# Kernel tuning notes

Hardware: AMD Instinct MI355X
Metric: run time of the kernel (lower is better)

## Reference

```python
import jax, jax.numpy as jnp
import numpy as np
import math

HIDDEN = 768
HEADS = 12
HEAD_DIM = HIDDEN // HEADS
BLOCK = 256
TOPK = 3
BATCH = 2
SEQ = 2048


def setup_inputs() -> dict:
    key = jax.random.key(0)
    ks = jax.random.split(key, 5)
    s = 1.0 / math.sqrt(HIDDEN)
    return {
        "hidden_states": jax.random.normal(ks[0], (BATCH, SEQ, HIDDEN), jnp.float32),
        "Wq": jax.random.normal(ks[1], (HIDDEN, HIDDEN), jnp.float32) * s,
        "Wk": jax.random.normal(ks[2], (HIDDEN, HIDDEN), jnp.float32) * s,
        "Wv": jax.random.normal(ks[3], (HIDDEN, HIDDEN), jnp.float32) * s,
        "Wo": jax.random.normal(ks[4], (HIDDEN, HIDDEN), jnp.float32) * s,
    }


def _rope(x, sin, cos):
    # x: [B, H, S, D]; rotate-half RoPE
    d2 = x.shape[-1] // 2
    x1, x2 = x[..., :d2], x[..., d2:]
    return x * cos + jnp.concatenate([-x2, x1], axis=-1) * sin


def reference(hidden_states, Wq, Wk, Wv, Wo):
    B, S, Hd = hidden_states.shape
    H, D, bs, K = HEADS, HEAD_DIM, BLOCK, TOPK
    nb = S // bs  # number of key blocks
    scale = 1.0 / math.sqrt(D)

    def split_heads(x):
        return x.reshape(B, S, H, D).transpose(0, 2, 1, 3)  # [B,H,S,D]

    q = split_heads(hidden_states @ Wq.T)
    k = split_heads(hidden_states @ Wk.T)
    v = split_heads(hidden_states @ Wv.T)

    # rotary embedding (standard rotate-half RoPE, base 10000)
    inv_freq = 1.0 / (10000.0 ** (jnp.arange(0, D, 2, dtype=jnp.float32) / D))
    ang = jnp.arange(S, dtype=jnp.float32)[:, None] * inv_freq[None, :]  # [S, D/2]
    emb = jnp.concatenate([ang, ang], axis=-1)  # [S, D]
    sin, cos = jnp.sin(emb), jnp.cos(emb)
    q = _rope(q, sin, cos)
    k = _rope(k, sin, cos)

    # mean-pooled block representations of keys: [B,H,nb,D]
    block_reps = k.reshape(B, H, nb, bs, D).mean(axis=3)

    # routing scores: per-token score against each block rep
    bscores = jnp.einsum('bhsd,bhnd->bhsn', q, block_reps) * scale  # [B,H,S,nb]
    pos = jnp.arange(S)
    cur = pos // bs                       # current block of each query, [S]
    blk = jnp.arange(nb)
    future = blk[None, None, None, :] > cur[None, None, :, None]
    bscores = jnp.where(future, -jnp.inf, bscores)
    # current block is force-selected (score set to dtype max)
    is_cur = blk[None, None, None, :] == cur[None, None, :, None]
    bscores = jnp.where(is_cur, jnp.finfo(bscores.dtype).max, bscores)

    _, topk_idx = jax.lax.top_k(bscores, min(K, nb))  # [B,H,S,K]
    selected = jnp.sum(jax.nn.one_hot(topk_idx, nb, dtype=jnp.float32), axis=-2) > 0  # [B,H,S,nb]

    # per-key-position mask: key t allowed iff its block is selected for query i,
    # and within the current block only t <= i (matches original truncation).
    sel_t = selected[:, :, :, cur]                          # [B,H,Sq,Sk]
    intra_ok = (cur[None, :] != cur[:, None]) | (pos[None, :] <= pos[:, None])  # [Sq,Sk]
    mask = sel_t & intra_ok[None, None]

    scores = jnp.einsum('bhqd,bhkd->bhqk', q, k) * scale
    scores = jnp.where(mask, scores, -jnp.inf)
    probs = jax.nn.softmax(scores, axis=-1)
    out = jnp.einsum('bhqk,bhkd->bhqd', probs, v)

    out = out.transpose(0, 2, 1, 3).reshape(B, S, Hd)
    return out @ Wo.T
```

## Files before the change

### kernel.cpp

```cpp
#include <hip/hip_runtime.h>
#include <math.h>


#define HID   768
#define NH    12
#define DH    64
#define SEQN  2048
#define BATCH 2
#define NTOK  (BATCH*SEQN)
#define NB    8
#define BLKSZ 256
#define NEG_INF (-__builtin_huge_valf())
#define POS_INF (__builtin_huge_valf())
#define LO_SCALE 2048.0f
#define LO_INV   (1.0f/2048.0f)
#define EXP2C    0.18033688f

typedef unsigned short u16;
typedef _Float16 v8hf __attribute__((ext_vector_type(8)));
typedef float    v4f  __attribute__((ext_vector_type(4)));

__device__ __forceinline__ u16 f2h(float x) {
    _Float16 h = (_Float16)x;
    return __builtin_bit_cast(u16, h);
}
__device__ __forceinline__ float h2f(u16 u) {
    return (float)__builtin_bit_cast(_Float16, u);
}
__device__ __forceinline__ v8hf ldhf8(const u16* p) {
    return *reinterpret_cast<const v8hf*>(p);
}
__device__ __forceinline__ void g2lds16(const u16* g, u16* l) {
    __builtin_amdgcn_global_load_lds(
        (const __attribute__((address_space(1))) void*)g,
        (__attribute__((address_space(3))) void*)l, 16, 0, 0);
}
#define MFMA16(a, b, c) __builtin_amdgcn_mfma_f32_16x16x32_f16(a, b, c, 0, 0, 0)

__global__ __launch_bounds__(256)
void preproc_k(const float* __restrict__ X,  const float* __restrict__ Wq,
               const float* __restrict__ Wk, const float* __restrict__ Wv,
               const float* __restrict__ Wo, float2* __restrict__ tab,
               u16* __restrict__ Xh, u16* __restrict__ Xl,
               u16* __restrict__ Wq2, u16* __restrict__ Wk2,
               u16* __restrict__ Wv2, u16* __restrict__ Wo2)
{
    const int NW = HID * HID;
    const int id = blockIdx.x;
    const int tid = threadIdx.x;
    if (id < 12288) {
        const int i = id * 256 + tid;
        const float x = X[i];
        const u16 h = f2h(x);
        Xh[i] = h;
        Xl[i] = f2h((x - h2f(h)) * LO_SCALE);
    } else if (id < 21504) {
        const int j = (id - 12288) * 256 + tid;
        const int z = j / NW, i = j - z * NW;
        const float* src = (z == 0) ? Wq : (z == 1) ? Wk : (z == 2) ? Wv : Wo;
        u16* dst = (z == 0) ? Wq2 : (z == 1) ? Wk2 : (z == 2) ? Wv2 : Wo2;
        const float x = src[i];
        const u16 h = f2h(x);
        dst[i] = h;
        dst[i + NW] = f2h((x - h2f(h)) * LO_SCALE);
    } else {
        const int i = (id - 21504) * 256 + tid;
        const int s = i >> 5, f = i & 31;
        const double y  = exp((double)f * (log(10000.0) / 32.0));
        const float yf = (float)y;
        const float invf = 1.0f / yf;
        const float ang  = (float)s * invf;
        tab[i] = make_float2((float)sin((double)ang), (float)cos((double)ang));
    }
}

__device__ __forceinline__
void qkv_mainloop(const u16* __restrict__ Ah, const u16* __restrict__ Al,
                  const u16* __restrict__ Bh, const u16* __restrict__ Bl,
                  int m0, int nb0, int c_start,
                  u16* As, u16* Bs, v4f acc[2][4])
{
    const int tid = threadIdx.x;
    const int w = tid >> 6, lane = tid & 63;
    const int col = lane & 15, quad = lane >> 4;

    int a_row[4], a_gl[4];
    #pragma unroll
    for (int r = 0; r < 4; r++) {
        const int g = r * 256 + tid;
        a_row[r] = g >> 3;
        a_gl[r]  = (g & 7) ^ (a_row[r] & 7);
    }
    int b_row[2], b_gl[2];
    #pragma unroll
    for (int r = 0; r < 2; r++) {
        const int g = r * 256 + tid;
        b_row[r] = g >> 3;
        b_gl[r]  = (g & 7) ^ (b_row[r] & 7);
    }

    for (int c = c_start; c < 3; c++) {
        const u16* Ap = (c == 0) ? Al : Ah;
        const u16* Bp = (c == 1) ? Bl : Bh;
        for (int itc = 0; itc < HID / 64; itc++) {
            const int k0 = itc * 64;
            __syncthreads();
            #pragma unroll
            for (int r = 0; r < 4; r++)
                g2lds16(Ap + (size_t)(m0 + a_row[r]) * HID + k0 + a_gl[r] * 8,
                        &As[(r * 256 + w * 64) * 8]);
            #pragma unroll
            for (int r = 0; r < 2; r++)
                g2lds16(Bp + (size_t)(nb0 + b_row[r]) * HID + k0 + b_gl[r] * 8,
                        &Bs[(r * 256 + w * 64) * 8]);
            __syncthreads();
            #pragma unroll
            for (int ks = 0; ks < 2; ks++) {
                v8hf af[2], bf_[4];
                #pragma unroll
                for (int mt = 0; mt < 2; mt++) {
                    const int row = w * 32 + mt * 16 + col;
                    const int gph = (ks * 4 + quad) ^ (row & 7);
                    af[mt] = ldhf8(&As[row * 64 + gph * 8]);
                }
                #pragma unroll
                for (int nt = 0; nt < 4; nt++) {
                    const int row = nt * 16 + col;
                    const int gph = (ks * 4 + quad) ^ (row & 7);
                    bf_[nt] = ldhf8(&Bs[row * 64 + gph * 8]);
                }
                #pragma unroll
                for (int mt = 0; mt < 2; mt++)
                    #pragma unroll
                    for (int nt = 0; nt < 4; nt++)
                        acc[mt][nt] = MFMA16(af[mt], bf_[nt], acc[mt][nt]);
            }
        }
        if (c == 1) {
            #pragma unroll
            for (int mt = 0; mt < 2; mt++)
                #pragma unroll
                for (int nt = 0; nt < 4; nt++)
                    #pragma unroll
                    for (int r = 0; r < 4; r++)
                        acc[mt][nt][r] *= LO_INV;
        }
    }
    __syncthreads();
}

__global__ __launch_bounds__(256)
void qkv_fused_gemm_k(const u16* __restrict__ Xh, const u16* __restrict__ Xl,
                      const u16* __restrict__ Wq2, const u16* __restrict__ Wk2,
                      const u16* __restrict__ Wv2, const float2* __restrict__ tab,
                      float* __restrict__ q32, u16* __restrict__ kh16,
                      u16* __restrict__ vth, float* __restrict__ partial)
{
    __shared__ u16 As[128 * 64];
    __shared__ u16 Bs[64 * 64];
    __shared__ float psum[4][64];

    const int NW = HID * HID;
    const int id    = blockIdx.x;
    const int xcd   = id & 7, loc = id >> 3;
    const int mtile = xcd * 4 + (loc & 3);
    const int ntile = loc >> 2;
    const int m0  = mtile * 128;
    const int mat = ntile / 12;
    const int nb0 = (ntile - mat * 12) * 64;
    const u16* Bh = (mat == 0) ? Wq2 : (mat == 1) ? Wk2 : Wv2;

    v4f acc[2][4] = {};
    qkv_mainloop(Xh, Xl, Bh, Bh + NW, m0, nb0, (mat == 2) ? 1 : 0, As, Bs, acc);

    const int tid = threadIdx.x;
    const int w = tid >> 6, lane = tid & 63;
    const int col = lane & 15, quad = lane >> 4;
    const int b = m0 >> 11;
    const int h = nb0 >> 6;
    const size_t bh = (size_t)b * NH + h;

    if (mat == 2) {
        #pragma unroll
        for (int nt = 0; nt < 4; nt++) {
            const int d = nt * 16 + col;
            #pragma unroll
            for (int mt = 0; mt < 2; mt++) {
                const int m = m0 + w * 32 + mt * 16 + quad * 4;
                const int s = m & (SEQN - 1);
                ushort4 pk = make_ushort4(f2h(acc[mt][nt][0]), f2h(acc[mt][nt][1]),
                                          f2h(acc[mt][nt][2]), f2h(acc[mt][nt][3]));
                *(ushort4*)&vth[(bh * DH + d) * SEQN + s] = pk;
            }
        }
        return;
    }

    float vsum[4] = {0.f, 0.f, 0.f, 0.f};
    #pragma unroll
    for (int mt = 0; mt < 2; mt++) {
        #pragma unroll
        for (int nt = 0; nt < 4; nt++) {
            const int d = nt * 16 + col;
            #pragma unroll
            for (int r = 0; r < 4; r++) {
                const int m = m0 + w * 32 + mt * 16 + quad * 4 + r;
                const int s = m & (SEQN - 1);
                const float part = acc[mt][nt ^ 2][r];
                const float2 sc = tab[(s << 5) + (d & 31)];
                const float val = (d < 32) ? acc[mt][nt][r] * sc.y - part * sc.x
                                           : acc[mt][nt][r] * sc.y + part * sc.x;
                const size_t idx = (bh * SEQN + s) * DH + d;
                if (mat == 0) {
                    q32[idx] = val;
                } else {
                    kh16[idx] = f2h(val);
                    vsum[nt] += val;
                }
            }
        }
    }
    if (mat == 1) {
        #pragma unroll
        for (int nt = 0; nt < 4; nt++) {
            float v = vsum[nt];
            v += __shfl_xor(v, 16);
            v += __shfl_xor(v, 32);
            if (quad == 0) psum[w][nt * 16 + col] = v;
        }
        __syncthreads();
        if (tid < 64) {
            const float s4 = (psum[0][tid] + psum[1][tid])
                           + (psum[2][tid] + psum[3][tid]);
            const int nblk = (m0 & (SEQN - 1)) >> 8;
            const int half = (m0 >> 7) & 1;
            partial[((bh * NB + nblk) * 2 + half) * 64 + tid] = s4;
        }
    }
}

__global__ __launch_bounds__(256)
void out_gemm_mfma_k(const u16* __restrict__ Ah, const u16* __restrict__ Wo2,
                     float* __restrict__ C)
{
    __shared__ u16 As[64 * 64];
    __shared__ u16 Bs[64 * 64];

    const int NW = HID * HID;
    const int id    = blockIdx.x;
    const int xcd   = id & 7, loc = id >> 3;
    const int mtile = xcd * 8 + (loc & 7);
    const int ntile = loc >> 3;
    const int m0 = mtile * 64, n0 = ntile * 64;
    const int tid = threadIdx.x;
    const int w = tid >> 6, lane = tid & 63;
    const int col = lane & 15, quad = lane >> 4;

    const int r0 = tid >> 3,         gl0 = (tid & 7) ^ (r0 & 7);
    const int r1 = (256 + tid) >> 3, gl1 = ((256 + tid) & 7) ^ (r1 & 7);

    v4f acc[4] = {};
    #pragma unroll
    for (int c = 0; c < 2; c++) {
        const u16* Bp = (c == 0) ? (Wo2 + NW) : Wo2;
        for (int itc = 0; itc < HID / 64; itc++) {
            const int k0 = itc * 64;
            __syncthreads();
            g2lds16(Ah + (size_t)(m0 + r0) * HID + k0 + gl0 * 8, &As[(w * 64) * 8]);
            g2lds16(Ah + (size_t)(m0 + r1) * HID + k0 + gl1 * 8, &As[(256 + w * 64) * 8]);
            g2lds16(Bp + (size_t)(n0 + r0) * HID + k0 + gl0 * 8, &Bs[(w * 64) * 8]);
            g2lds16(Bp + (size_t)(n0 + r1) * HID + k0 + gl1 * 8, &Bs[(256 + w * 64) * 8]);
            __syncthreads();
            #pragma unroll
            for (int ks = 0; ks < 2; ks++) {
                const int arow = w * 16 + col;
                v8hf a = ldhf8(&As[arow * 64 + (((ks * 4 + quad) ^ (arow & 7))) * 8]);
                #pragma unroll
                for (int nt = 0; nt < 4; nt++) {
                    const int row = nt * 16 + col;
                    v8hf bb = ldhf8(&Bs[row * 64 + (((ks * 4 + quad) ^ (row & 7))) * 8]);
                    acc[nt] = MFMA16(a, bb, acc[nt]);
                }
            }
        }
        if (c == 0) {
            #pragma unroll
            for (int nt = 0; nt < 4; nt++)
                #pragma unroll
                for (int r = 0; r < 4; r++)
                    acc[nt][r] *= LO_INV;
        }
    }

    #pragma unroll
    for (int nt = 0; nt < 4; nt++)
        #pragma unroll
        for (int r = 0; r < 4; r++) {
            const int m = m0 + w * 16 + quad * 4 + r;
            C[(size_t)m * HID + n0 + nt * 16 + col] = acc[nt][r];
        }
}

__global__ __launch_bounds__(64)
void reps_reduce_k(const float* __restrict__ partial, float* __restrict__ reps)
{
    const int bhn = blockIdx.x;
    const int d = threadIdx.x;
    const float* p = &partial[(size_t)bhn * 128 + d];
    double s = (double)p[0] + (double)p[64];
    reps[(size_t)bhn * 64 + d] = (float)(s * (1.0 / 256.0));
}

__global__ __launch_bounds__(128)
void select_topk_k(const float* __restrict__ qg, const float* __restrict__ reps,
                   unsigned* __restrict__ selm)
{
    __shared__ float rs[NB][DH];
    const int bh = blockIdx.y;
    const int tid = threadIdx.x;
    for (int idx = tid; idx < NB * DH; idx += 128)
        rs[idx >> 6][idx & 63] = reps[(size_t)bh * NB * DH + idx];
    __syncthreads();

    const int qq = blockIdx.x * 128 + tid;
    const float* qv = &qg[((size_t)bh * SEQN + qq) * DH];
    float qr[DH];
    #pragma unroll
    for (int c = 0; c < 16; c++) {
        float4 t = *(const float4*)&qv[c * 4];
        qr[c*4+0]=t.x; qr[c*4+1]=t.y; qr[c*4+2]=t.z; qr[c*4+3]=t.w;
    }
    const int cur = qq >> 8;
    double sc[NB];
    #pragma unroll
    for (int n = 0; n < NB; n++) {
        double ssum = 0.0;
        for (int d = 0; d < DH; d++) ssum += (double)qr[d] * (double)rs[n][d];
        sc[n] = ssum * 0.125;
    }
    for (int n = cur + 1; n < NB; n++) sc[n] = -1e300;
    sc[cur] = 1e300;
    unsigned mask = 0;
    for (int p = 0; p < 3; p++) {
        int bi = -1; double bv = 0.0;
        for (int n = 0; n < NB; n++) {
            if ((mask >> n) & 1) continue;
            if (bi < 0 || sc[n] > bv) { bi = n; bv = sc[n]; }
        }
        mask |= 1u << bi;
    }
    selm[(size_t)bh * SEQN + qq] = mask;
}

__global__ __launch_bounds__(256, 4)
void moba_attn_k(const float* __restrict__ q32, const u16* __restrict__ kh16,
                 const u16* __restrict__ vth, const unsigned* __restrict__ selm,
                 u16* __restrict__ aoh)
{
    __shared__ u16 kbuf[2][64 * 64];
    __shared__ u16 vbuf[2][64 * 64];
    __shared__ u16 plds[4][16][64];
    unsigned* s_uni = (unsigned*)&vbuf[1][0];

    const int id  = blockIdx.x;
    const int xcd = id & 7, loc = id >> 3;
    const int bh  = xcd * 3 + (loc >> 5);
    const int q0  = (loc & 31) * 64;
    const int cur = q0 >> 8;
    const int tid = threadIdx.x;
    const int wave = tid >> 6, lane = tid & 63;
    const int col = lane & 15, quad = lane >> 4;
    const int qw0 = q0 + wave * 16;
    const int qpos = qw0 + col;
    const size_t bhS = (size_t)bh * SEQN;
    const size_t bhV = (size_t)bh * DH;

    if (tid == 0) *s_uni = 0;
    __syncthreads();
    const unsigned mymask = selm[bhS + qw0 + col];
    unsigned uw = mymask;
    #pragma unroll
    for (int off = 1; off < 16; off <<= 1) uw |= __shfl_xor(uw, off);
    if (lane == 0) atomicOr(s_uni, uw);

    v8hf qh[2], ql[2];
    #pragma unroll
    for (int ks = 0; ks < 2; ks++) {
        const float* qp = &q32[(bhS + qw0 + col) * DH + ks * 32 + quad * 8];
        float4 f0 = *(const float4*)qp;
        float4 f1 = *(const float4*)(qp + 4);
        float qf[8] = {f0.x, f0.y, f0.z, f0.w, f1.x, f1.y, f1.z, f1.w};
        union { u16 u[8]; v8hf h; } uh, ul;
        #pragma unroll
        for (int j = 0; j < 8; j++) {
            u16 hb = f2h(qf[j]);
            uh.u[j] = hb;
            ul.u[j] = f2h((qf[j] - h2f(hb)) * LO_SCALE);
        }
        qh[ks] = uh.h; ql[ks] = ul.h;
    }
    __syncthreads();
    const unsigned uni = __builtin_amdgcn_readfirstlane(*s_uni);

    int n_cur = __builtin_ctz(uni), c_cur = 0;
    int n_nxt = n_cur, c_nxt = 0;
    bool has_nxt = true;
    auto c2max = [&](int n) { return (n == cur) ? ((q0 + 63 - n * BLKSZ) >> 6) : 3; };
    auto advance = [&]() {
        if (c_nxt < c2max(n_nxt)) { c_nxt++; return; }
        has_nxt = false;
        for (int nn = n_nxt + 1; nn < NB; nn++)
            if ((uni >> nn) & 1) { n_nxt = nn; c_nxt = 0; has_nxt = true; return; }
    };
    advance();

    const int sg_row0 = tid >> 3;
    const int sg_gl0  = (tid & 7) ^ (sg_row0 & 7);
    const int sg_row1 = (256 + tid) >> 3;
    const int sg_gl1  = ((256 + tid) & 7) ^ (sg_row1 & 7);
    auto stage = [&](int n, int c2, int buf) {
        const int kb = n * BLKSZ + c2 * 64;
        u16* kd = (u16*)kbuf[buf];
        u16* vd = (u16*)vbuf[buf];
        const size_t ks0 = (bhS + kb + sg_row0) * DH + sg_gl0 * 8;
        const size_t ks1 = (bhS + kb + sg_row1) * DH + sg_gl1 * 8;
        const size_t vs0 = (bhV + sg_row0) * SEQN + kb + sg_gl0 * 8;
        const size_t vs1 = (bhV + sg_row1) * SEQN + kb + sg_gl1 * 8;
        g2lds16(kh16 + ks0, kd + (wave * 64) * 8);
        g2lds16(kh16 + ks1, kd + (256 + wave * 64) * 8);
        g2lds16(vth + vs0, vd + (wave * 64) * 8);
        g2lds16(vth + vs1, vd + (256 + wave * 64) * 8);
    };

    const v4f zero4 = {0.f, 0.f, 0.f, 0.f};
    v4f oacc[4] = {zero4, zero4, zero4, zero4};
    float m_i = NEG_INF, l_i = 0.f;
    const int psw = (col & 7) << 1;

    stage(n_cur, c_cur, 0);
    int t = 0;
    while (true) {
        __syncthreads();
        if (has_nxt) stage(n_nxt, c_nxt, (t + 1) & 1);

        const int n  = n_cur;
        const int kb = n * BLKSZ + c_cur * 64;
        const bool iscur = (n == cur);
        const float selinf = ((mymask >> n) & 1) ? 0.f : POS_INF;
        const bool need_mask = iscur && (kb + 63 > qw0);
        const u16* kd = (const u16*)kbuf[t & 1];
        const u16* vd = (const u16*)vbuf[t & 1];

        v4f sf[4];
        #pragma unroll
        for (int mt = 0; mt < 4; mt++) {
            const int row = mt * 16 + col;
            const int r7 = row & 7;
            v8hf kh0 = ldhf8(&kd[(row * 8 + (quad ^ r7)) * 8]);
            v8hf kh1 = ldhf8(&kd[(row * 8 + ((4 + quad) ^ r7)) * 8]);
            v4f c = zero4;
            c = MFMA16(kh0, ql[0], c);
            c = MFMA16(kh1, ql[1], c);
            #pragma unroll
            for (int r = 0; r < 4; r++) c[r] *= LO_INV;
            c = MFMA16(kh0, qh[0], c);
            c = MFMA16(kh1, qh[1], c);
            sf[mt] = c;
        }

        if (need_mask) {
            #pragma unroll
            for (int mt = 0; mt < 4; mt++)
                #pragma unroll
                for (int r = 0; r < 4; r++) {
                    const int kidx = kb + mt * 16 + quad * 4 + r;
                    sf[mt][r] = (kidx <= qpos) ? sf[mt][r] : NEG_INF;
                }
        }

        float rm = NEG_INF;
        #pragma unroll
        for (int mt = 0; mt < 4; mt++)
            #pragma unroll
            for (int r = 0; r < 4; r++) rm = fmaxf(rm, sf[mt][r]);
        rm = fmaxf(rm, __shfl_xor(rm, 16));
        rm = fmaxf(rm, __shfl_xor(rm, 32));
        rm = rm - selinf;
        const float mnew  = fmaxf(m_i, rm);
        const float alpha = (m_i == NEG_INF) ? 0.f : exp2f((m_i - mnew) * EXP2C);
        const float biasC = ((mnew == NEG_INF) ? 0.f : mnew * EXP2C) + selinf;

        float lsum = 0.f;
        #pragma unroll
        for (int mt = 0; mt < 4; mt++) {
            ushort4 hv;
            #pragma unroll
            for (int r = 0; r < 4; r++) {
                float p = exp2f(fmaf(sf[mt][r], EXP2C, -biasC));
                lsum += p;
                u16 hu = f2h(p);
                if (r == 0) hv.x = hu;
                else if (r == 1) hv.y = hu;
                else if (r == 2) hv.z = hu;
                else hv.w = hu;
            }
            *(ushort4*)&plds[wave][col][((mt * 4 + quad) ^ psw) * 4] = hv;
        }
        lsum += __shfl_xor(lsum, 16);
        lsum += __shfl_xor(lsum, 32);
        l_i = l_i * alpha + lsum;
        m_i = mnew;

        float ar[4];
        #pragma unroll
        for (int r = 0; r < 4; r++) ar[r] = __shfl(alpha, quad * 4 + r, 16);
        #pragma unroll
        for (int nt = 0; nt < 4; nt++)
            #pragma unroll
            for (int r = 0; r < 4; r++) oacc[nt][r] *= ar[r];

        __threadfence_block();

        #pragma unroll
        for (int ks2 = 0; ks2 < 2; ks2++) {
            v8hf ph = ldhf8(&plds[wave][col][((ks2 * 8 + quad * 2) ^ psw) * 4]);
            #pragma unroll
            for (int nt = 0; nt < 4; nt++) {
                const int row = nt * 16 + col;
                const int g = (ks2 * 4 + quad) ^ (row & 7);
                v8hf vh = ldhf8(&vd[(row * 8 + g) * 8]);
                oacc[nt] = MFMA16(ph, vh, oacc[nt]);
            }
        }

        if (!has_nxt) break;
        n_cur = n_nxt; c_cur = c_nxt;
        advance();
        t++;
    }

    const int b = bh / NH, h = bh % NH;
    const float invl = 1.f / l_i;
    float ir[4];
    #pragma unroll
    for (int r = 0; r < 4; r++) ir[r] = __shfl(invl, quad * 4 + r, 16);
    #pragma unroll
    for (int nt = 0; nt < 4; nt++)
        #pragma unroll
        for (int r = 0; r < 4; r++) {
            const int qi = qw0 + quad * 4 + r;
            const size_t idx = ((size_t)b * SEQN + qi) * HID + h * DH + nt * 16 + col;
            aoh[idx] = f2h(oacc[nt][r] * ir[r]);
        }
}

extern "C" void kernel_launch(void* const* d_in, const int* in_sizes, int n_in,
                              void* d_out, int out_size, void* d_ws, size_t ws_size,
                              hipStream_t stream)
{
    const float* X  = (const float*)d_in[0];
    const float* Wq = (const float*)d_in[1];
    const float* Wk = (const float*)d_in[2];
    const float* Wv = (const float*)d_in[3];
    const float* Wo = (const float*)d_in[4];
    float* out = (float*)d_out;

    char* p = (char*)d_ws;
    float* q32 = (float*)p;                p += (size_t)NTOK*HID*4;
    u16* kh16 = (u16*)p;                   p += (size_t)NTOK*HID*2;
    u16* vth  = (u16*)p;                   p += (size_t)NTOK*HID*2;
    u16* Xh   = (u16*)p;                   p += (size_t)NTOK*HID*2;
    u16* Xl   = (u16*)p;                   p += (size_t)NTOK*HID*2;
    u16* Wq2  = (u16*)p;                   p += (size_t)HID*HID*2*2;
    u16* Wk2  = (u16*)p;                   p += (size_t)HID*HID*2*2;
    u16* Wv2  = (u16*)p;                   p += (size_t)HID*HID*2*2;
    u16* Wo2  = (u16*)p;                   p += (size_t)HID*HID*2*2;
    float* partial = (float*)p;            p += (size_t)BATCH*NH*NB*2*64*4;
    float* reps    = (float*)p;            p += (size_t)BATCH*NH*NB*DH*4;
    unsigned* selm = (unsigned*)p;         p += (size_t)BATCH*NH*SEQN*4;
    float2* tab    = (float2*)p;           p += (size_t)SEQN*32*8;
    u16* aoh = Xh;

    preproc_k<<<dim3(21760), 256, 0, stream>>>(X, Wq, Wk, Wv, Wo, tab,
                                               Xh, Xl, Wq2, Wk2, Wv2, Wo2);

    qkv_fused_gemm_k<<<dim3(1152), 256, 0, stream>>>(
        Xh, Xl, Wq2, Wk2, Wv2, tab, q32, kh16, vth, partial);

    reps_reduce_k<<<dim3(BATCH*NH*NB), 64, 0, stream>>>(partial, reps);
    select_topk_k<<<dim3(SEQN/128, BATCH*NH), 128, 0, stream>>>(q32, reps, selm);

    moba_attn_k<<<dim3(BATCH*NH*(SEQN/64)), 256, 0, stream>>>(
        q32, kh16, vth, selm, aoh);

    out_gemm_mfma_k<<<dim3(768), 256, 0, stream>>>(aoh, Wo2, out);
}
```

Measured before the change: 235.5 us.

## Split attention KV loop for late query blocks and merge partials in combine kernel

```diff
diff --git a/kernel.cpp b/kernel.cpp
--- a/kernel.cpp
+++ b/kernel.cpp
@@ -15,6 +15,9 @@
 #define LO_SCALE 2048.0f
 #define LO_INV   (1.0f/2048.0f)
 #define EXP2C    0.18033688f
+
+#define SPLIT_ROWS 1024
+#define NBH   (BATCH*NH)
 
 typedef unsigned short u16;
 typedef _Float16 v8hf __attribute__((ext_vector_type(8)));
@@ -355,7 +358,8 @@
 __global__ __launch_bounds__(256, 4)
 void moba_attn_k(const float* __restrict__ q32, const u16* __restrict__ kh16,
                  const u16* __restrict__ vth, const unsigned* __restrict__ selm,
-                 u16* __restrict__ aoh)
+                 u16* __restrict__ aoh, float* __restrict__ po,
+                 float* __restrict__ ml)
 {
     __shared__ u16 kbuf[2][64 * 64];
     __shared__ u16 vbuf[2][64 * 64];
@@ -364,8 +368,12 @@
 
     const int id  = blockIdx.x;
     const int xcd = id & 7, loc = id >> 3;
-    const int bh  = xcd * 3 + (loc >> 5);
-    const int q0  = (loc & 31) * 64;
+    const int bh  = xcd * 3 + loc / 48;
+    const int u   = loc % 48;
+    int qb, split, stride;
+    if (u < 16) { qb = u;                 split = 0;          stride = 1; }
+    else        { qb = 16 + ((u - 16) >> 1); split = (u - 16) & 1; stride = 2; }
+    const int q0  = qb * 64;
     const int cur = q0 >> 8;
     const int tid = threadIdx.x;
     const int wave = tid >> 6, lane = tid & 63;
@@ -382,6 +390,7 @@
     #pragma unroll
     for (int off = 1; off < 16; off <<= 1) uw |= __shfl_xor(uw, off);
     if (lane == 0) atomicOr(s_uni, uw);
+    const unsigned wmask = __builtin_amdgcn_readfirstlane(uw);
 
     v8hf qh[2], ql[2];
     #pragma unroll
@@ -402,17 +411,39 @@
     __syncthreads();
     const unsigned uni = __builtin_amdgcn_readfirstlane(*s_uni);
 
-    int n_cur = __builtin_ctz(uni), c_cur = 0;
-    int n_nxt = n_cur, c_nxt = 0;
+    int n_nxt = __builtin_ctz(uni), c_nxt = 0;
     bool has_nxt = true;
     auto c2max = [&](int n) { return (n == cur) ? ((q0 + 63 - n * BLKSZ) >> 6) : 3; };
-    auto advance = [&]() {
+    auto advance1 = [&]() {
         if (c_nxt < c2max(n_nxt)) { c_nxt++; return; }
+        for (int nn = n_nxt + 1; nn < NB; nn++)
+            if ((uni >> nn) & 1) { n_nxt = nn; c_nxt = 0; return; }
         has_nxt = false;
-        for (int nn = n_nxt + 1; nn < NB; nn++)
-            if ((uni >> nn) & 1) { n_nxt = nn; c_nxt = 0; has_nxt = true; return; }
     };
-    advance();
+    for (int i = 0; i < split; i++) if (has_nxt) advance1();
+    int n_cur = n_nxt, c_cur = c_nxt;
+    const bool cur_valid = has_nxt;
+
+    const size_t srow0 = (size_t)bh * SPLIT_ROWS + (q0 - SPLIT_ROWS);
+
+    if (!cur_valid) {
+        if (stride == 2) {
+            if (quad == 0) {
+                const size_t r = srow0 + wave * 16 + col;
+                ml[(r * 2 + split) * 2 + 0] = NEG_INF;
+                ml[(r * 2 + split) * 2 + 1] = 0.f;
+            }
+            #pragma unroll
+            for (int nt = 0; nt < 4; nt++)
+                #pragma unroll
+                for (int r = 0; r < 4; r++) {
+                    const size_t rq = srow0 + wave * 16 + quad * 4 + r;
+                    po[(rq * 2 + split) * 64 + nt * 16 + col] = 0.f;
+                }
+        }
+        return;
+    }
+    for (int i = 0; i < stride; i++) if (has_nxt) advance1();
 
     const int sg_row0 = tid >> 3;
     const int sg_gl0  = (tid & 7) ^ (sg_row0 & 7);
@@ -444,99 +475,121 @@
         if (has_nxt) stage(n_nxt, c_nxt, (t + 1) & 1);
 
         const int n  = n_cur;
-        const int kb = n * BLKSZ + c_cur * 64;
-        const bool iscur = (n == cur);
-        const float selinf = ((mymask >> n) & 1) ? 0.f : POS_INF;
-        const bool need_mask = iscur && (kb + 63 > qw0);
-        const u16* kd = (const u16*)kbuf[t & 1];
-        const u16* vd = (const u16*)vbuf[t & 1];
-
-        v4f sf[4];
-        #pragma unroll
-        for (int mt = 0; mt < 4; mt++) {
-            const int row = mt * 16 + col;
-            const int r7 = row & 7;
-            v8hf kh0 = ldhf8(&kd[(row * 8 + (quad ^ r7)) * 8]);
-            v8hf kh1 = ldhf8(&kd[(row * 8 + ((4 + quad) ^ r7)) * 8]);
-            v4f c = zero4;
-            c = MFMA16(kh0, ql[0], c);
-            c = MFMA16(kh1, ql[1], c);
-            #pragma unroll
-            for (int r = 0; r < 4; r++) c[r] *= LO_INV;
-            c = MFMA16(kh0, qh[0], c);
-            c = MFMA16(kh1, qh[1], c);
-            sf[mt] = c;
-        }
-
-        if (need_mask) {
+        if ((wmask >> n) & 1) {
+            const int kb = n * BLKSZ + c_cur * 64;
+            const bool iscur = (n == cur);
+            const float selinf = ((mymask >> n) & 1) ? 0.f : POS_INF;
+            const bool need_mask = iscur && (kb + 63 > qw0);
+            const u16* kd = (const u16*)kbuf[t & 1];
+            const u16* vd = (const u16*)vbuf[t & 1];
+
+            v4f sf[4];
+            __builtin_amdgcn_s_setprio(1);
+            #pragma unroll
+            for (int mt = 0; mt < 4; mt++) {
+                const int row = mt * 16 + col;
+                const int r7 = row & 7;
+                v8hf kh0 = ldhf8(&kd[(row * 8 + (quad ^ r7)) * 8]);
+                v8hf kh1 = ldhf8(&kd[(row * 8 + ((4 + quad) ^ r7)) * 8]);
+                v4f c = zero4;
+                c = MFMA16(kh0, ql[0], c);
+                c = MFMA16(kh1, ql[1], c);
+                #pragma unroll
+                for (int r = 0; r < 4; r++) c[r] *= LO_INV;
+                c = MFMA16(kh0, qh[0], c);
+                c = MFMA16(kh1, qh[1], c);
+                sf[mt] = c;
+            }
+            __builtin_amdgcn_s_setprio(0);
+
+            if (need_mask) {
+                #pragma unroll
+                for (int mt = 0; mt < 4; mt++)
+                    #pragma unroll
+                    for (int r = 0; r < 4; r++) {
+                        const int kidx = kb + mt * 16 + quad * 4 + r;
+                        sf[mt][r] = (kidx <= qpos) ? sf[mt][r] : NEG_INF;
+                    }
+            }
+
+            float rm = NEG_INF;
             #pragma unroll
             for (int mt = 0; mt < 4; mt++)
                 #pragma unroll
+                for (int r = 0; r < 4; r++) rm = fmaxf(rm, sf[mt][r]);
+            rm = fmaxf(rm, __shfl_xor(rm, 16));
+            rm = fmaxf(rm, __shfl_xor(rm, 32));
+            rm = rm - selinf;
+            const float mnew  = fmaxf(m_i, rm);
+            const float alpha = (m_i == NEG_INF) ? 0.f : exp2f((m_i - mnew) * EXP2C);
+            const float biasC = ((mnew == NEG_INF) ? 0.f : mnew * EXP2C) + selinf;
+
+            float lsum = 0.f;
+            #pragma unroll
+            for (int mt = 0; mt < 4; mt++) {
+                ushort4 hv;
+                #pragma unroll
                 for (int r = 0; r < 4; r++) {
-                    const int kidx = kb + mt * 16 + quad * 4 + r;
-                    sf[mt][r] = (kidx <= qpos) ? sf[mt][r] : NEG_INF;
+                    float p = exp2f(fmaf(sf[mt][r], EXP2C, -biasC));
+                    lsum += p;
+                    u16 hu = f2h(p);
+                    if (r == 0) hv.x = hu;
+                    else if (r == 1) hv.y = hu;
+                    else if (r == 2) hv.z = hu;
+                    else hv.w = hu;
                 }
-        }
-
-        float rm = NEG_INF;
-        #pragma unroll
-        for (int mt = 0; mt < 4; mt++)
-            #pragma unroll
-            for (int r = 0; r < 4; r++) rm = fmaxf(rm, sf[mt][r]);
-        rm = fmaxf(rm, __shfl_xor(rm, 16));
-        rm = fmaxf(rm, __shfl_xor(rm, 32));
-        rm = rm - selinf;
-        const float mnew  = fmaxf(m_i, rm);
-        const float alpha = (m_i == NEG_INF) ? 0.f : exp2f((m_i - mnew) * EXP2C);
-        const float biasC = ((mnew == NEG_INF) ? 0.f : mnew * EXP2C) + selinf;
-
-        float lsum = 0.f;
-        #pragma unroll
-        for (int mt = 0; mt < 4; mt++) {
-            ushort4 hv;
-            #pragma unroll
-            for (int r = 0; r < 4; r++) {
-                float p = exp2f(fmaf(sf[mt][r], EXP2C, -biasC));
-                lsum += p;
-                u16 hu = f2h(p);
-                if (r == 0) hv.x = hu;
-                else if (r == 1) hv.y = hu;
-                else if (r == 2) hv.z = hu;
-                else hv.w = hu;
-            }
-            *(ushort4*)&plds[wave][col][((mt * 4 + quad) ^ psw) * 4] = hv;
-        }
-        lsum += __shfl_xor(lsum, 16);
-        lsum += __shfl_xor(lsum, 32);
-        l_i = l_i * alpha + lsum;
-        m_i = mnew;
-
-        float ar[4];
-        #pragma unroll
-        for (int r = 0; r < 4; r++) ar[r] = __shfl(alpha, quad * 4 + r, 16);
+                *(ushort4*)&plds[wave][col][((mt * 4 + quad) ^ psw) * 4] = hv;
+            }
+            lsum += __shfl_xor(lsum, 16);
+            lsum += __shfl_xor(lsum, 32);
+            l_i = l_i * alpha + lsum;
+            m_i = mnew;
+
+            float ar[4];
+            #pragma unroll
+            for (int r = 0; r < 4; r++) ar[r] = __shfl(alpha, quad * 4 + r, 16);
+            #pragma unroll
+            for (int nt = 0; nt < 4; nt++)
+                #pragma unroll
+                for (int r = 0; r < 4; r++) oacc[nt][r] *= ar[r];
+
+            __threadfence_block();
+
+            __builtin_amdgcn_s_setprio(1);
+            #pragma unroll
+            for (int ks2 = 0; ks2 < 2; ks2++) {
+                v8hf ph = ldhf8(&plds[wave][col][((ks2 * 8 + quad * 2) ^ psw) * 4]);
+                #pragma unroll
+                for (int nt = 0; nt < 4; nt++) {
+                    const int row = nt * 16 + col;
+                    const int g = (ks2 * 4 + quad) ^ (row & 7);
+                    v8hf vh = ldhf8(&vd[(row * 8 + g) * 8]);
+                    oacc[nt] = MFMA16(ph, vh, oacc[nt]);
+                }
+            }
+            __builtin_amdgcn_s_setprio(0);
+        }
+
+        if (!has_nxt) break;
+        n_cur = n_nxt; c_cur = c_nxt;
+        for (int i = 0; i < stride; i++) if (has_nxt) advance1();
+        t++;
+    }
+
+    if (stride == 2) {
+        if (quad == 0) {
+            const size_t r = srow0 + wave * 16 + col;
+            ml[(r * 2 + split) * 2 + 0] = m_i;
+            ml[(r * 2 + split) * 2 + 1] = l_i;
+        }
         #pragma unroll
         for (int nt = 0; nt < 4; nt++)
             #pragma unroll
-            for (int r = 0; r < 4; r++) oacc[nt][r] *= ar[r];
-
-        __threadfence_block();
-
-        #pragma unroll
-        for (int ks2 = 0; ks2 < 2; ks2++) {
-            v8hf ph = ldhf8(&plds[wave][col][((ks2 * 8 + quad * 2) ^ psw) * 4]);
-            #pragma unroll
-            for (int nt = 0; nt < 4; nt++) {
-                const int row = nt * 16 + col;
-                const int g = (ks2 * 4 + quad) ^ (row & 7);
-                v8hf vh = ldhf8(&vd[(row * 8 + g) * 8]);
-                oacc[nt] = MFMA16(ph, vh, oacc[nt]);
-            }
-        }
-
-        if (!has_nxt) break;
-        n_cur = n_nxt; c_cur = c_nxt;
-        advance();
-        t++;
+            for (int r = 0; r < 4; r++) {
+                const size_t rq = srow0 + wave * 16 + quad * 4 + r;
+                po[(rq * 2 + split) * 64 + nt * 16 + col] = oacc[nt][r];
+            }
+        return;
     }
 
     const int b = bh / NH, h = bh % NH;
@@ -552,6 +605,28 @@
             const size_t idx = ((size_t)b * SEQN + qi) * HID + h * DH + nt * 16 + col;
             aoh[idx] = f2h(oacc[nt][r] * ir[r]);
         }
+}
+
+__global__ __launch_bounds__(256)
+void attn_combine_k(const float* __restrict__ po, const float* __restrict__ ml,
+                    u16* __restrict__ aoh)
+{
+    const int g = blockIdx.x * 256 + threadIdx.x;
+    const int d = g & 63;
+    const size_t row = (size_t)(g >> 6);
+    const int bh = (int)(row >> 10);
+    const int qlocal = (int)(row & 1023);
+    const float m0 = ml[(row * 2 + 0) * 2 + 0], l0 = ml[(row * 2 + 0) * 2 + 1];
+    const float m1 = ml[(row * 2 + 1) * 2 + 0], l1 = ml[(row * 2 + 1) * 2 + 1];
+    const float m  = fmaxf(m0, m1);
+    const float a0 = (m0 == NEG_INF) ? 0.f : exp2f((m0 - m) * EXP2C);
+    const float a1 = (m1 == NEG_INF) ? 0.f : exp2f((m1 - m) * EXP2C);
+    const float o  = po[(row * 2 + 0) * 64 + d] * a0
+                   + po[(row * 2 + 1) * 64 + d] * a1;
+    const float inv = 1.f / (l0 * a0 + l1 * a1);
+    const int b = bh / NH, h = bh % NH;
+    const int q = SPLIT_ROWS + qlocal;
+    aoh[((size_t)b * SEQN + q) * HID + h * DH + d] = f2h(o * inv);
 }
 
 extern "C" void kernel_launch(void* const* d_in, const int* in_sizes, int n_in,
@@ -581,6 +656,9 @@
     float2* tab    = (float2*)p;           p += (size_t)SEQN*32*8;
     u16* aoh = Xh;
 
+    float* po = (float*)Xl;
+    float* ml = po + (size_t)NBH * SPLIT_ROWS * 2 * 64;
+
     preproc_k<<<dim3(21760), 256, 0, stream>>>(X, Wq, Wk, Wv, Wo, tab,
                                                Xh, Xl, Wq2, Wk2, Wv2, Wo2);
 
@@ -590,8 +668,10 @@
     reps_reduce_k<<<dim3(BATCH*NH*NB), 64, 0, stream>>>(partial, reps);
     select_topk_k<<<dim3(SEQN/128, BATCH*NH), 128, 0, stream>>>(q32, reps, selm);
 
-    moba_attn_k<<<dim3(BATCH*NH*(SEQN/64)), 256, 0, stream>>>(
-        q32, kh16, vth, selm, aoh);
+    moba_attn_k<<<dim3(1152), 256, 0, stream>>>(
+        q32, kh16, vth, selm, aoh, po, ml);
+
+    attn_combine_k<<<dim3(6144), 256, 0, stream>>>(po, ml, aoh);
 
     out_gemm_mfma_k<<<dim3(768), 256, 0, stream>>>(aoh, Wo2, out);
 }
```

Measured after the change: 227.0 us. 3.6% less time.
